# Optimization experiments

Hardware: AMD Instinct MI355X
Metric: run time of the kernel (lower is better)

The kernel has to match this reference:

```python
import jax, jax.numpy as jnp
import numpy as np

EPS = 1e-5

def _ln(x, g, b):
    mu = jnp.mean(x, axis=-1, keepdims=True)
    var = jnp.var(x, axis=-1, keepdims=True)
    return (x - mu) * jax.lax.rsqrt(var + EPS) * g + b

def setup_inputs() -> dict:
    key = jax.random.key(0)
    ks = jax.random.split(key, 8)
    B, N, D, H = 1, 512, 128, 128
    s = 1.0 / np.sqrt(D)
    inp = {
        'x': jax.random.normal(ks[0], (B, N, N, D), dtype=jnp.float32),
        'src_mask': jax.random.randint(ks[1], (B, N), 0, 2, dtype=jnp.int32),
        'ln_g': jnp.ones((D,), jnp.float32), 'ln_b': jnp.zeros((D,), jnp.float32),
        'Wl': jax.random.normal(ks[2], (D, H), jnp.float32) * s,
        'bl': jnp.zeros((H,), jnp.float32),
        'Wr': jax.random.normal(ks[3], (D, H), jnp.float32) * s,
        'br': jnp.zeros((H,), jnp.float32),
        # gates: faithful to nn.init.constant_(weight, 0.), constant_(bias, 1.)
        'Wlg': jnp.zeros((D, H), jnp.float32), 'blg': jnp.ones((H,), jnp.float32),
        'Wrg': jnp.zeros((D, H), jnp.float32), 'brg': jnp.ones((H,), jnp.float32),
        'Wog': jnp.zeros((D, H), jnp.float32), 'bog': jnp.ones((H,), jnp.float32),
        'oln_g': jnp.ones((H,), jnp.float32), 'oln_b': jnp.zeros((H,), jnp.float32),
        'Wo': jax.random.normal(ks[4], (H, D), jnp.float32) / np.sqrt(H),
        'bo': jnp.zeros((D,), jnp.float32),
    }
    return inp

def reference(x, src_mask, ln_g, ln_b, Wl, bl, Wr, br, Wlg, blg, Wrg, brg, Wog, bog, oln_g, oln_b, Wo, bo):
    # pairwise mask (B,i,j,1) = outer product of src_mask with itself
    m = src_mask.astype(jnp.float32)
    mask = (m[:, :, None] * m[:, None, :])[..., None]
    xn = _ln(x, ln_g, ln_b)
    # original applies left/right proj to detached xn (no grad to x via these paths)
    xd = jax.lax.stop_gradient(xn)
    left = (xd @ Wl + bl) * mask
    right = (xd @ Wr + br) * mask
    left = left * jax.nn.sigmoid(xn @ Wlg + blg)
    right = right * jax.nn.sigmoid(xn @ Wrg + brg)
    out_gate = jax.nn.sigmoid(xn @ Wog + bog)
    # ingoing mix: '... k j d, ... k i d -> ... i j d'
    out = jnp.einsum('bkjd,bkid->bijd', left, right)
    out = _ln(out, oln_g, oln_b) * out_gate
    return out @ Wo + bo
```

## Files before the change

kernel.cpp:

```cpp
#include <hip/hip_runtime.h>
#include <stdint.h>

#define NN 512
#define PP (NN * NN)

typedef __attribute__((ext_vector_type(8))) short bf16x8;
typedef __attribute__((ext_vector_type(4))) float f32x4;

#define MFMA16 __builtin_amdgcn_mfma_f32_16x16x32_bf16

__device__ __forceinline__ unsigned short f2bf(float f) {
  unsigned u = __float_as_uint(f);
  u += 0x7fffu + ((u >> 16) & 1u);
  return (unsigned short)(u >> 16);
}
__device__ __forceinline__ float bf2f(unsigned short s) {
  return __uint_as_float(((unsigned)s) << 16);
}
__device__ __forceinline__ unsigned pack2(float a, float b) {
  return (unsigned)f2bf(a) | ((unsigned)f2bf(b) << 16);
}
__device__ __forceinline__ float sigm(float t) { return 1.0f / (1.0f + __expf(-t)); }

__device__ __forceinline__ int sidx(int p, int h) {
  return p * 136 + (h ^ (((p >> 3) & 7) << 3));
}

__global__ __launch_bounds__(256) void k_prep(
    const float* __restrict__ w0, const float* __restrict__ w1,
    const float* __restrict__ w2, const float* __restrict__ w3,
    const float* __restrict__ w4, const float* __restrict__ w5,
    unsigned short* __restrict__ outw) {
  const float* src;
  switch (blockIdx.x) {
    case 0: src = w0; break; case 1: src = w1; break; case 2: src = w2; break;
    case 3: src = w3; break; case 4: src = w4; break; default: src = w5; break;
  }
  unsigned short* o = outw + blockIdx.x * 16384;
  for (int idx = threadIdx.x; idx < 16384; idx += 256) {
    int r = idx >> 7, c = idx & 127;
    o[idx] = f2bf(src[c * 128 + r]);
  }
}

__global__ __launch_bounds__(256) void k_ln(
    const float* __restrict__ x, const float* __restrict__ g,
    const float* __restrict__ b, unsigned short* __restrict__ xn) {
  const int lane = threadIdx.x & 63, wid = threadIdx.x >> 6;
  const int row = blockIdx.x * 32 + wid * 8 + (lane >> 3);
  const int ch = lane & 7;
  const float4* xr = (const float4*)(x + (size_t)row * 128 + ch * 16);
  float4 V[4];
  float s = 0.f, ss = 0.f;
#pragma unroll
  for (int q = 0; q < 4; ++q) {
    V[q] = xr[q];
    s  += V[q].x + V[q].y + V[q].z + V[q].w;
    ss += V[q].x * V[q].x + V[q].y * V[q].y + V[q].z * V[q].z + V[q].w * V[q].w;
  }
#pragma unroll
  for (int o = 1; o < 8; o <<= 1) { s += __shfl_xor(s, o); ss += __shfl_xor(ss, o); }
  float mu  = s * 0.0078125f;
  float var = ss * 0.0078125f - mu * mu;
  float rs  = rsqrtf(var + 1e-5f);
  const float4* gp = (const float4*)(g + ch * 16);
  const float4* bp = (const float4*)(b + ch * 16);
  unsigned pk[8];
#pragma unroll
  for (int q = 0; q < 4; ++q) {
    float4 vv = V[q], gg = gp[q], bb = bp[q];
    pk[2 * q]     = pack2((vv.x - mu) * rs * gg.x + bb.x, (vv.y - mu) * rs * gg.y + bb.y);
    pk[2 * q + 1] = pack2((vv.z - mu) * rs * gg.z + bb.z, (vv.w - mu) * rs * gg.w + bb.w);
  }
  unsigned short* dst = xn + (size_t)row * 128 + ch * 16;
  *(uint4*)dst       = make_uint4(pk[0], pk[1], pk[2], pk[3]);
  *(uint4*)(dst + 8) = make_uint4(pk[4], pk[5], pk[6], pk[7]);
}

__global__ __launch_bounds__(256) void k_proj(
    const unsigned short* __restrict__ xn,
    const unsigned short* __restrict__ WpT, const float* __restrict__ bp,
    const unsigned short* __restrict__ WgT, const float* __restrict__ bg,
    const int* __restrict__ mask,
    unsigned short* __restrict__ outb) {
  const int c  = blockIdx.y;
  const int k0 = blockIdx.x * 128;
  const int t = threadIdx.x, lane = t & 63, wid = t >> 6;
  const int wm = (wid >> 1) * 64, wn = (wid & 1) * 64;
  const int lr = lane & 15, lg = lane >> 4;
  __shared__ unsigned short sX[128 * 136];
  __shared__ unsigned short sW[128 * 136];

#pragma unroll
  for (int it = 0; it < 8; ++it) {
    int lin = it * 256 + t;
    int r = lin >> 4, ch = lin & 15;
    *(uint4*)&sX[r * 136 + ch * 8] =
        *(const uint4*)&xn[((size_t)(k0 + r) * NN + c) * 128 + ch * 8];
  }
#pragma unroll
  for (int it = 0; it < 8; ++it) {
    int lin = it * 256 + t;
    *(uint4*)&sW[(lin >> 4) * 136 + (lin & 15) * 8] = *(const uint4*)&WgT[lin * 8];
  }
  __syncthreads();

  f32x4 acc[4][4];
#pragma unroll
  for (int m = 0; m < 4; ++m)
#pragma unroll
    for (int n = 0; n < 4; ++n) { acc[m][n][0] = 0.f; acc[m][n][1] = 0.f; acc[m][n][2] = 0.f; acc[m][n][3] = 0.f; }

#pragma unroll
  for (int kk = 0; kk < 4; ++kk) {
    bf16x8 av[4], bv[4];
#pragma unroll
    for (int m = 0; m < 4; ++m)
      av[m] = *(const bf16x8*)&sW[(wm + m * 16 + lr) * 136 + kk * 32 + lg * 8];
#pragma unroll
    for (int n = 0; n < 4; ++n)
      bv[n] = *(const bf16x8*)&sX[(wn + n * 16 + lr) * 136 + kk * 32 + lg * 8];
#pragma unroll
    for (int m = 0; m < 4; ++m)
#pragma unroll
      for (int n = 0; n < 4; ++n)
        acc[m][n] = MFMA16(av[m], bv[n], acc[m][n], 0, 0, 0);
  }
  float sg[4][4][4];
#pragma unroll
  for (int m = 0; m < 4; ++m)
#pragma unroll
    for (int r = 0; r < 4; ++r) {
      int h = wm + m * 16 + lg * 4 + r;
      float bgv = bg[h];
#pragma unroll
      for (int n = 0; n < 4; ++n) sg[m][n][r] = sigm(acc[m][n][r] + bgv);
    }
  __syncthreads();
#pragma unroll
  for (int it = 0; it < 8; ++it) {
    int lin = it * 256 + t;
    *(uint4*)&sW[(lin >> 4) * 136 + (lin & 15) * 8] = *(const uint4*)&WpT[lin * 8];
  }
  __syncthreads();

#pragma unroll
  for (int m = 0; m < 4; ++m)
#pragma unroll
    for (int n = 0; n < 4; ++n) { acc[m][n][0] = 0.f; acc[m][n][1] = 0.f; acc[m][n][2] = 0.f; acc[m][n][3] = 0.f; }
#pragma unroll
  for (int kk = 0; kk < 4; ++kk) {
    bf16x8 av[4], bv[4];
#pragma unroll
    for (int m = 0; m < 4; ++m)
      av[m] = *(const bf16x8*)&sW[(wm + m * 16 + lr) * 136 + kk * 32 + lg * 8];
#pragma unroll
    for (int n = 0; n < 4; ++n)
      bv[n] = *(const bf16x8*)&sX[(wn + n * 16 + lr) * 136 + kk * 32 + lg * 8];
#pragma unroll
    for (int m = 0; m < 4; ++m)
#pragma unroll
      for (int n = 0; n < 4; ++n)
        acc[m][n] = MFMA16(av[m], bv[n], acc[m][n], 0, 0, 0);
  }

  const int maskc = mask[c];
  float mcol[4];
#pragma unroll
  for (int n = 0; n < 4; ++n)
    mcol[n] = (float)(maskc * mask[k0 + wn + n * 16 + lr]);
#pragma unroll
  for (int m = 0; m < 4; ++m)
#pragma unroll
    for (int r = 0; r < 4; ++r) {
      int h = wm + m * 16 + lg * 4 + r;
      float bpv = bp[h];
#pragma unroll
      for (int n = 0; n < 4; ++n) {
        float v = (acc[m][n][r] + bpv) * mcol[n] * sg[m][n][r];
        outb[(size_t)h * PP + (size_t)c * NN + k0 + wn + n * 16 + lr] = f2bf(v);
      }
    }
}

__global__ __launch_bounds__(512) void k_einsum(
    const unsigned short* __restrict__ rightT,
    const unsigned short* __restrict__ leftT,
    unsigned short* __restrict__ tmp) {
  const int bid = (blockIdx.x & 7) * 64 + (blockIdx.x >> 3);
  const int d = bid >> 2;
  const int i0 = ((bid >> 1) & 1) * 256, j0 = (bid & 1) * 256;
  const unsigned short* A = rightT + (size_t)d * PP;
  const unsigned short* B = leftT + (size_t)d * PP;
  const int t = threadIdx.x, lane = t & 63, wid = t >> 6;
  const int wm = (wid >> 2) * 128, wn = (wid & 3) * 64;
  const int lr = lane & 15, lg = lane >> 4;
  __shared__ unsigned short sA[256 * 72];
  __shared__ unsigned short sB[256 * 72];

  f32x4 acc[8][4];
#pragma unroll
  for (int m = 0; m < 8; ++m)
#pragma unroll
    for (int n = 0; n < 4; ++n) { acc[m][n][0] = 0.f; acc[m][n][1] = 0.f; acc[m][n][2] = 0.f; acc[m][n][3] = 0.f; }

  for (int kb = 0; kb < 8; ++kb) {
#pragma unroll
    for (int it = 0; it < 4; ++it) {
      int lin = it * 512 + t;
      int r = lin >> 3, ch = lin & 7;
      *(uint4*)&sA[r * 72 + ch * 8] =
          *(const uint4*)&A[(size_t)(i0 + r) * NN + kb * 64 + ch * 8];
      *(uint4*)&sB[r * 72 + ch * 8] =
          *(const uint4*)&B[(size_t)(j0 + r) * NN + kb * 64 + ch * 8];
    }
    __syncthreads();
#pragma unroll
    for (int kk = 0; kk < 2; ++kk) {
      bf16x8 bv[4];
#pragma unroll
      for (int n = 0; n < 4; ++n)
        bv[n] = *(const bf16x8*)&sB[(wn + n * 16 + lr) * 72 + kk * 32 + lg * 8];
#pragma unroll
      for (int m = 0; m < 8; ++m) {
        bf16x8 av = *(const bf16x8*)&sA[(wm + m * 16 + lr) * 72 + kk * 32 + lg * 8];
#pragma unroll
        for (int n = 0; n < 4; ++n)
          acc[m][n] = MFMA16(av, bv[n], acc[m][n], 0, 0, 0);
      }
    }
    __syncthreads();
  }
#pragma unroll
  for (int m = 0; m < 8; ++m)
#pragma unroll
    for (int r = 0; r < 4; ++r) {
      int row = wm + m * 16 + lg * 4 + r;
#pragma unroll
      for (int n = 0; n < 4; ++n) {
        int col = wn + n * 16 + lr;
        tmp[(size_t)d * PP + (size_t)(i0 + row) * NN + j0 + col] = f2bf(acc[m][n][r]);
      }
    }
}

__global__ __launch_bounds__(256, 2) void k_final(
    const unsigned short* __restrict__ xn,
    const unsigned short* __restrict__ WogT, const float* __restrict__ bog,
    const unsigned short* __restrict__ WoT, const float* __restrict__ bo,
    const unsigned short* __restrict__ tmp,
    const float* __restrict__ og, const float* __restrict__ ob,
    float* __restrict__ out) {
  const int p0 = blockIdx.x * 128;
  const int t = threadIdx.x, lane = t & 63, wid = t >> 6;
  const int wm = (wid >> 1) * 64, wn = (wid & 1) * 64;
  const int lr = lane & 15, lg = lane >> 4;
  __shared__ unsigned short sT[128 * 136];
  __shared__ unsigned short sSig[128 * 136];
  __shared__ float muL[128], rsL[128];

  {
    const int pb = 2 * lane;
#pragma unroll
    for (int q = 0; q < 4; ++q) {
      int h0 = (q * 4 + wid) * 8;
      unsigned a[8];
#pragma unroll
      for (int e = 0; e < 8; ++e)
        a[e] = *(const unsigned*)&tmp[(size_t)(h0 + e) * PP + p0 + pb];
      bf16x8 y0, y1;
#pragma unroll
      for (int e = 0; e < 8; ++e) {
        y0[e] = (short)(a[e] & 0xffffu);
        y1[e] = (short)(a[e] >> 16);
      }
      *(bf16x8*)&sT[sidx(pb, h0)]     = y0;
      *(bf16x8*)&sT[sidx(pb + 1, h0)] = y1;
    }
  }

  f32x4 acc[4][4];
#pragma unroll
  for (int m = 0; m < 4; ++m)
#pragma unroll
    for (int n = 0; n < 4; ++n) { acc[m][n][0] = 0.f; acc[m][n][1] = 0.f; acc[m][n][2] = 0.f; acc[m][n][3] = 0.f; }
#pragma unroll
  for (int kk = 0; kk < 4; ++kk) {
    bf16x8 av[4], bv[4];
#pragma unroll
    for (int m = 0; m < 4; ++m)
      av[m] = *(const bf16x8*)&xn[(size_t)(p0 + wm + m * 16 + lr) * 128 + kk * 32 + lg * 8];
#pragma unroll
    for (int n = 0; n < 4; ++n)
      bv[n] = *(const bf16x8*)&WogT[(wn + n * 16 + lr) * 128 + kk * 32 + lg * 8];
#pragma unroll
    for (int m = 0; m < 4; ++m)
#pragma unroll
      for (int n = 0; n < 4; ++n)
        acc[m][n] = MFMA16(av[m], bv[n], acc[m][n], 0, 0, 0);
  }
  float bogv[4];
#pragma unroll
  for (int n = 0; n < 4; ++n) bogv[n] = bog[wn + n * 16 + lr];
#pragma unroll
  for (int m = 0; m < 4; ++m)
#pragma unroll
    for (int r = 0; r < 4; ++r) {
      int p = wm + m * 16 + lg * 4 + r;
#pragma unroll
      for (int n = 0; n < 4; ++n)
        sSig[sidx(p, wn + n * 16 + lr)] = f2bf(sigm(acc[m][n][r] + bogv[n]));
    }
  __syncthreads();

  {
    int p = t >> 1, half = t & 1;
    float s = 0.f, ss = 0.f;
#pragma unroll
    for (int c = 0; c < 8; ++c) {
      bf16x8 v = *(const bf16x8*)&sT[sidx(p, half * 64 + c * 8)];
#pragma unroll
      for (int e = 0; e < 8; ++e) {
        float f = bf2f((unsigned short)v[e]);
        s += f; ss += f * f;
      }
    }
    s += __shfl_xor(s, 1); ss += __shfl_xor(ss, 1);
    if (half == 0) {
      float mu = s * 0.0078125f;
      float var = ss * 0.0078125f - mu * mu;
      muL[p] = mu;
      rsL[p] = rsqrtf(var + 1e-5f);
    }
  }
  __syncthreads();

#pragma unroll
  for (int m = 0; m < 4; ++m)
#pragma unroll
    for (int n = 0; n < 4; ++n) { acc[m][n][0] = 0.f; acc[m][n][1] = 0.f; acc[m][n][2] = 0.f; acc[m][n][3] = 0.f; }
  float muR[4], rsR[4];
#pragma unroll
  for (int m = 0; m < 4; ++m) {
    int p = wm + m * 16 + lr;
    muR[m] = muL[p]; rsR[m] = rsL[p];
  }
#pragma unroll
  for (int kk = 0; kk < 4; ++kk) {
    const int h0 = kk * 32 + lg * 8;
    float ogv[8], obv[8];
    *(float4*)&ogv[0] = *(const float4*)&og[h0];
    *(float4*)&ogv[4] = *(const float4*)&og[h0 + 4];
    *(float4*)&obv[0] = *(const float4*)&ob[h0];
    *(float4*)&obv[4] = *(const float4*)&ob[h0 + 4];
    bf16x8 av[4], bv[4];
#pragma unroll
    for (int m = 0; m < 4; ++m) {
      int p = wm + m * 16 + lr;
      float mu = muR[m], rr = rsR[m];
      bf16x8 tv = *(const bf16x8*)&sT[sidx(p, h0)];
      bf16x8 gv = *(const bf16x8*)&sSig[sidx(p, h0)];
      bf16x8 y;
#pragma unroll
      for (int e = 0; e < 8; ++e) {
        float tf = bf2f((unsigned short)tv[e]);
        float yf = ((tf - mu) * rr * ogv[e] + obv[e]) * bf2f((unsigned short)gv[e]);
        y[e] = (short)f2bf(yf);
      }
      av[m] = y;
    }
#pragma unroll
    for (int n = 0; n < 4; ++n)
      bv[n] = *(const bf16x8*)&WoT[(wn + n * 16 + lr) * 128 + h0];
#pragma unroll
    for (int m = 0; m < 4; ++m)
#pragma unroll
      for (int n = 0; n < 4; ++n)
        acc[m][n] = MFMA16(av[m], bv[n], acc[m][n], 0, 0, 0);
  }

  float bov[4];
#pragma unroll
  for (int n = 0; n < 4; ++n) bov[n] = bo[wn + n * 16 + lr];
#pragma unroll
  for (int m = 0; m < 4; ++m)
#pragma unroll
    for (int r = 0; r < 4; ++r) {
      int p = wm + m * 16 + lg * 4 + r;
#pragma unroll
      for (int n = 0; n < 4; ++n)
        out[(size_t)(p0 + p) * 128 + wn + n * 16 + lr] = acc[m][n][r] + bov[n];
    }
}

extern "C" void kernel_launch(void* const* d_in, const int* in_sizes, int n_in,
                              void* d_out, int out_size, void* d_ws, size_t ws_size,
                              hipStream_t stream) {
  (void)in_sizes; (void)n_in; (void)out_size;
  const float* x    = (const float*)d_in[0];
  const int*   msk  = (const int*)d_in[1];
  const float* ln_g = (const float*)d_in[2];
  const float* ln_b = (const float*)d_in[3];
  const float* Wl   = (const float*)d_in[4];
  const float* bl   = (const float*)d_in[5];
  const float* Wr   = (const float*)d_in[6];
  const float* br   = (const float*)d_in[7];
  const float* Wlg  = (const float*)d_in[8];
  const float* blg  = (const float*)d_in[9];
  const float* Wrg  = (const float*)d_in[10];
  const float* brg  = (const float*)d_in[11];
  const float* Wog  = (const float*)d_in[12];
  const float* bog  = (const float*)d_in[13];
  const float* olng = (const float*)d_in[14];
  const float* olnb = (const float*)d_in[15];
  const float* Wo   = (const float*)d_in[16];
  const float* bo   = (const float*)d_in[17];
  float* out = (float*)d_out;

  const size_t need = (1ull << 20) + 4ull * (1ull << 26);
  if (ws_size < need) return;
  char* ws = (char*)d_ws;
  unsigned short* wT    = (unsigned short*)ws;
  unsigned short* xn    = (unsigned short*)(ws + (1ull << 20));
  unsigned short* leftT = (unsigned short*)(ws + (1ull << 20) + (1ull << 26));
  unsigned short* rightT= (unsigned short*)(ws + (1ull << 20) + (2ull << 26));
  unsigned short* tmp   = (unsigned short*)(ws + (1ull << 20) + (3ull << 26));

  hipLaunchKernelGGL(k_prep, dim3(6), dim3(256), 0, stream, Wl, Wr, Wlg, Wrg, Wog, Wo, wT);
  hipLaunchKernelGGL(k_ln, dim3(PP / 32), dim3(256), 0, stream, x, ln_g, ln_b, xn);
  hipLaunchKernelGGL(k_proj, dim3(4, NN), dim3(256), 0, stream,
                     xn, wT + 0 * 16384, bl, wT + 2 * 16384, blg, msk, leftT);
  hipLaunchKernelGGL(k_proj, dim3(4, NN), dim3(256), 0, stream,
                     xn, wT + 1 * 16384, br, wT + 3 * 16384, brg, msk, rightT);
  hipLaunchKernelGGL(k_einsum, dim3(512), dim3(512), 0, stream, rightT, leftT, tmp);
  hipLaunchKernelGGL(k_final, dim3(PP / 128), dim3(256), 0, stream,
                     xn, wT + 4 * 16384, bog, wT + 5 * 16384, bo, tmp, olng, olnb, out);
}
```

Measured before the change: 274.5 us.

## Prefetch next K-tile into registers during MFMA compute in einsum kernel

The einsum kernel now loads the next 64-wide K slice of A and B from global memory into registers while the current slice is being multiplied from shared memory. After compute, it writes the registers into shared memory. This overlaps global load latency with MFMA work instead of serialising load, sync and compute. In exchange it uses 32 extra VGPRs per thread, which may increase register pressure in an already large accumulator tile (8x4 f32x4).

```diff
diff --git a/kernel.cpp b/kernel.cpp
--- a/kernel.cpp
+++ b/kernel.cpp
@@ -195,6 +195,8 @@
   const int t = threadIdx.x, lane = t & 63, wid = t >> 6;
   const int wm = (wid >> 2) * 128, wn = (wid & 3) * 64;
   const int lr = lane & 15, lg = lane >> 4;
+  const int sr = t >> 3;
+  const int sc = (t & 7) * 8;
   __shared__ unsigned short sA[256 * 72];
   __shared__ unsigned short sB[256 * 72];
 
@@ -204,17 +206,37 @@
 #pragma unroll
     for (int n = 0; n < 4; ++n) { acc[m][n][0] = 0.f; acc[m][n][1] = 0.f; acc[m][n][2] = 0.f; acc[m][n][3] = 0.f; }
 
+  uint4 pa0, pa1, pa2, pa3, pb0, pb1, pb2, pb3;
+  pa0 = *(const uint4*)&A[(size_t)(i0 + sr)       * NN + sc];
+  pa1 = *(const uint4*)&A[(size_t)(i0 + 64 + sr)  * NN + sc];
+  pa2 = *(const uint4*)&A[(size_t)(i0 + 128 + sr) * NN + sc];
+  pa3 = *(const uint4*)&A[(size_t)(i0 + 192 + sr) * NN + sc];
+  pb0 = *(const uint4*)&B[(size_t)(j0 + sr)       * NN + sc];
+  pb1 = *(const uint4*)&B[(size_t)(j0 + 64 + sr)  * NN + sc];
+  pb2 = *(const uint4*)&B[(size_t)(j0 + 128 + sr) * NN + sc];
+  pb3 = *(const uint4*)&B[(size_t)(j0 + 192 + sr) * NN + sc];
+  *(uint4*)&sA[(sr)       * 72 + sc] = pa0;
+  *(uint4*)&sA[(64 + sr)  * 72 + sc] = pa1;
+  *(uint4*)&sA[(128 + sr) * 72 + sc] = pa2;
+  *(uint4*)&sA[(192 + sr) * 72 + sc] = pa3;
+  *(uint4*)&sB[(sr)       * 72 + sc] = pb0;
+  *(uint4*)&sB[(64 + sr)  * 72 + sc] = pb1;
+  *(uint4*)&sB[(128 + sr) * 72 + sc] = pb2;
+  *(uint4*)&sB[(192 + sr) * 72 + sc] = pb3;
+  __syncthreads();
+
   for (int kb = 0; kb < 8; ++kb) {
-#pragma unroll
-    for (int it = 0; it < 4; ++it) {
-      int lin = it * 512 + t;
-      int r = lin >> 3, ch = lin & 7;
-      *(uint4*)&sA[r * 72 + ch * 8] =
-          *(const uint4*)&A[(size_t)(i0 + r) * NN + kb * 64 + ch * 8];
-      *(uint4*)&sB[r * 72 + ch * 8] =
-          *(const uint4*)&B[(size_t)(j0 + r) * NN + kb * 64 + ch * 8];
-    }
-    __syncthreads();
+    if (kb < 7) {
+      const int ko = (kb + 1) * 64 + sc;
+      pa0 = *(const uint4*)&A[(size_t)(i0 + sr)       * NN + ko];
+      pa1 = *(const uint4*)&A[(size_t)(i0 + 64 + sr)  * NN + ko];
+      pa2 = *(const uint4*)&A[(size_t)(i0 + 128 + sr) * NN + ko];
+      pa3 = *(const uint4*)&A[(size_t)(i0 + 192 + sr) * NN + ko];
+      pb0 = *(const uint4*)&B[(size_t)(j0 + sr)       * NN + ko];
+      pb1 = *(const uint4*)&B[(size_t)(j0 + 64 + sr)  * NN + ko];
+      pb2 = *(const uint4*)&B[(size_t)(j0 + 128 + sr) * NN + ko];
+      pb3 = *(const uint4*)&B[(size_t)(j0 + 192 + sr) * NN + ko];
+    }
 #pragma unroll
     for (int kk = 0; kk < 2; ++kk) {
       bf16x8 bv[4];
@@ -230,7 +252,19 @@
       }
     }
     __syncthreads();
-  }
+    if (kb < 7) {
+      *(uint4*)&sA[(sr)       * 72 + sc] = pa0;
+      *(uint4*)&sA[(64 + sr)  * 72 + sc] = pa1;
+      *(uint4*)&sA[(128 + sr) * 72 + sc] = pa2;
+      *(uint4*)&sA[(192 + sr) * 72 + sc] = pa3;
+      *(uint4*)&sB[(sr)       * 72 + sc] = pb0;
+      *(uint4*)&sB[(64 + sr)  * 72 + sc] = pb1;
+      *(uint4*)&sB[(128 + sr) * 72 + sc] = pb2;
+      *(uint4*)&sB[(192 + sr) * 72 + sc] = pb3;
+    }
+    __syncthreads();
+  }
+
 #pragma unroll
   for (int m = 0; m < 8; ++m)
 #pragma unroll
```

Result: no change. 270.1 us, median of 4 (-1.6%).
